# Kernel optimization log

Measured on AMD Instinct MI355X. Metric: run time of the kernel, lower is better.

## Reference

```python
import jax, jax.numpy as jnp
import numpy as np

ANCHOR_LENGTHS = jnp.array([1., 2., 3., 4., 5., 7., 9.], dtype=jnp.float32)  # A = 7


def make_anchors_1d(Lf):
    # anchors [Lf*A, 2] in feature coords, matching torch make_anchors_1d
    centers = jnp.arange(Lf, dtype=jnp.float32) + 0.5          # [Lf]
    c = centers[:, None]                                        # [Lf,1]
    w = ANCHOR_LENGTHS[None, :]                                 # [1,A]
    start = c - 0.5 * w
    end = c + 0.5 * w
    return jnp.stack(jnp.broadcast_arrays(start, end), axis=-1).reshape(-1, 2)


def setup_inputs() -> dict:
    key = jax.random.key(0)
    ks = jax.random.split(key, 4)
    B, C, Lf, A = 8, 512, 16384, 7
    feat = jax.random.normal(ks[0], (B, C, Lf), dtype=jnp.float32)
    conv_w = jax.random.normal(ks[1], (C, C, 3), dtype=jnp.float32) * 0.02
    conv_b = jnp.zeros((C,), dtype=jnp.float32)
    obj_w = jax.random.normal(ks[2], (A, C, 1), dtype=jnp.float32) * 0.02
    obj_b = jnp.zeros((A,), dtype=jnp.float32)
    reg_w = jax.random.normal(ks[3], (A * 2, C, 1), dtype=jnp.float32) * 0.02
    reg_b = jnp.zeros((A * 2,), dtype=jnp.float32)
    return {"feat": feat, "conv_w": conv_w, "conv_b": conv_b,
            "obj_w": obj_w, "obj_b": obj_b, "reg_w": reg_w, "reg_b": reg_b}


def reference(feat, conv_w, conv_b, obj_w, obj_b, reg_w, reg_b):
    B, C, Lf = feat.shape
    A = obj_w.shape[0]
    # conv1d k=3 pad=1 (NCH layout), + bias, relu
    h = jax.lax.conv_general_dilated(
        feat, conv_w, window_strides=(1,), padding=((1, 1),),
        dimension_numbers=("NCH", "OIH", "NCH"))
    h = jax.nn.relu(h + conv_b[None, :, None])                  # [B,C,Lf]
    # 1x1 heads as channel contractions
    obj = jnp.einsum("bcl,ac->bla", h, obj_w[:, :, 0]) + obj_b  # [B,Lf,A]
    reg = jnp.einsum("bcl,oc->blo", h, reg_w[:, :, 0]) + reg_b  # [B,Lf,2A]
    obj = obj.reshape(B, Lf * A)                                # [B,N]
    reg = reg.reshape(B, Lf, A, 2).reshape(B, Lf * A, 2)        # [B,N,2]
    anchors = make_anchors_1d(Lf)                               # [N,2]
    return obj, reg, anchors
```

## Files before the change

kernel.cpp:

```cpp
#include <hip/hip_runtime.h>
#include <hip/hip_bf16.h>
#include <stdint.h>

typedef __attribute__((ext_vector_type(8))) short bh8;
typedef __attribute__((ext_vector_type(4))) float f32x4;
typedef unsigned short u16;
typedef unsigned int u32;

#define B_    8
#define C_    512
#define LF    16384
#define KTOT  1536

#define P4_BYTES ((size_t)4 * B_ * 21 * LF * 4)
#define W2_OFF   P4_BYTES

#define OBJ_OFF  0
#define REG_OFF  917504
#define ANC_OFF  2752512

__device__ __forceinline__ u16 f2bf(float f) {
    u32 u = __float_as_uint(f);
    return (u16)((u + 0x7FFFu + ((u >> 16) & 1u)) >> 16);
}
__device__ __forceinline__ u32 pk2bf(float lo, float hi) {
    u32 r;
    asm("v_cvt_pk_bf16_f32 %0, %1, %2" : "=v"(r) : "v"(lo), "v"(hi));
    return r;
}
__device__ __forceinline__ void gload16(const u16* g, u16* l) {
    __builtin_amdgcn_global_load_lds(
        (const __attribute__((address_space(1))) void*)g,
        (__attribute__((address_space(3))) void*)l, 16, 0, 0);
}

__global__ void k_cast_w(const float* __restrict__ cw, u16* __restrict__ W2) {
    int i = blockIdx.x * 256 + threadIdx.x;
    if (i >= C_ * KTOT) return;
    int co = i / KTOT, r = i % KTOT;
    int t = r >> 9, rem = r & 511;
    int kc = rem >> 6, cc = rem & 63;
    int jl = (cc >> 3) ^ (co & 7);
    int ci = kc * 64 + jl * 8 + (cc & 7);
    W2[i] = f2bf(cw[(co * C_ + ci) * 3 + t]);
}

__global__ void k_anchors(float* __restrict__ out) {
    int l = blockIdx.x * 256 + threadIdx.x;
    if (l >= LF) return;
    const float AL[7] = {1.f, 2.f, 3.f, 4.f, 5.f, 7.f, 9.f};
    float c = (float)l + 0.5f;
    float* an = out + ANC_OFF + (size_t)l * 14;
#pragma unroll
    for (int a = 0; a < 7; ++a) {
        an[a * 2 + 0] = c - 0.5f * AL[a];
        an[a * 2 + 1] = c + 0.5f * AL[a];
    }
}

__global__ __launch_bounds__(256, 4) void k_conv_head(
    const float* __restrict__ feat, const u16* __restrict__ W2,
    const float* __restrict__ conv_b, const float* __restrict__ obj_w,
    const float* __restrict__ reg_w, float* __restrict__ P4) {
    __shared__ __align__(16) char smem[40960];
    u16* As = (u16*)smem;
    u16* Bs = (u16*)(smem + 16384);
    u16* Hs = (u16*)smem;
    u16* Wp = (u16*)(smem + 32768);

    const int tid = threadIdx.x;
    const int lane = tid & 63, wave = tid >> 6;
    const int wm = wave >> 1, wn = wave & 1;
    const int g = lane >> 4, cL = lane & 15;

    const int wg = (blockIdx.x & 7) * 512 + (blockIdx.x >> 3);
    const int mt = wg & 3;
    const int l0 = ((wg >> 2) & 127) * 128;
    const int b  = wg >> 9;
    const int co0 = mt * 128;

    const int cg   = tid & 15;
    const int lgrp = tid >> 4;
    const int arow = tid >> 3;
    const int acol = (tid & 7) * 8;
    const int swA = (cL & 7) << 3;

    f32x4 acc[4][4];
#pragma unroll
    for (int m = 0; m < 4; ++m)
#pragma unroll
        for (int n = 0; n < 4; ++n) acc[m][n] = {0.f, 0.f, 0.f, 0.f};

    for (int kc = 0; kc < 8; ++kc) {
        __syncthreads();
        {
            const float* fp = feat +
                ((size_t)(b * C_ + kc * 64 + cg * 4)) * LF + l0 + lgrp * 8;
#pragma unroll
            for (int h = 0; h < 2; ++h) {
                float4 v0 = *(const float4*)(fp + 0 * LF + h * 4);
                float4 v1 = *(const float4*)(fp + 1 * LF + h * 4);
                float4 v2 = *(const float4*)(fp + 2 * LF + h * 4);
                float4 v3 = *(const float4*)(fp + 3 * LF + h * 4);
#pragma unroll
                for (int e = 0; e < 4; ++e) {
                    const int r = 1 + lgrp * 8 + h * 4 + e;
                    uint2 pk;
                    pk.x = pk2bf(((const float*)&v0)[e], ((const float*)&v1)[e]);
                    pk.y = pk2bf(((const float*)&v2)[e], ((const float*)&v3)[e]);
                    *(uint2*)&Bs[r * 64 + ((cg * 4) ^ ((r & 7) << 3))] = pk;
                }
            }
        }
        if (tid < 128) {
            const int ci2 = tid >> 1;
            const int rr = (tid & 1) ? 129 : 0;
            const int l = l0 + rr - 1;
            float v = (l >= 0 && l < LF)
                          ? feat[((size_t)(b * C_ + kc * 64 + ci2)) * LF + l]
                          : 0.f;
            Bs[rr * 64 + (ci2 ^ ((rr & 7) << 3))] = f2bf(v);
        }
#pragma unroll
        for (int t = 0; t < 3; ++t) {
            if (t > 0) __syncthreads();
#pragma unroll
            for (int p = 0; p < 4; ++p) {
                const int row = p * 32 + arow;
                gload16(&W2[(size_t)(co0 + row) * KTOT + t * 512 + kc * 64 + acol],
                        &As[row * 64 + acol]);
            }
            __syncthreads();
            const int swB = ((cL + t) & 7) << 3;
#pragma unroll
            for (int kk = 0; kk < 2; ++kk) {
                const int ko = kk * 32 + g * 8;
                bh8 af[4], bfr[4];
#pragma unroll
                for (int m = 0; m < 4; ++m)
                    af[m] = *(const bh8*)&As[(wm * 64 + m * 16 + cL) * 64 + (ko ^ swA)];
#pragma unroll
                for (int n = 0; n < 4; ++n)
                    bfr[n] = *(const bh8*)&Bs[(wn * 64 + n * 16 + cL + t) * 64 + (ko ^ swB)];
#pragma unroll
                for (int m = 0; m < 4; ++m)
#pragma unroll
                    for (int n = 0; n < 4; ++n)
                        acc[m][n] = __builtin_amdgcn_mfma_f32_16x16x32_bf16(
                            af[m], bfr[n], acc[m][n], 0, 0, 0);
            }
        }
    }
    __syncthreads();

#pragma unroll
    for (int m = 0; m < 4; ++m) {
        const int co_b = wm * 64 + m * 16 + g * 4;
        const float b0_ = conv_b[co0 + co_b + 0];
        const float b1_ = conv_b[co0 + co_b + 1];
        const float b2_ = conv_b[co0 + co_b + 2];
        const float b3_ = conv_b[co0 + co_b + 3];
#pragma unroll
        for (int n = 0; n < 4; ++n) {
            const int l = wn * 64 + n * 16 + cL;
            f32x4 v = acc[m][n];
            uint2 pk;
            pk.x = pk2bf(fmaxf(v[0] + b0_, 0.f), fmaxf(v[1] + b1_, 0.f));
            pk.y = pk2bf(fmaxf(v[2] + b2_, 0.f), fmaxf(v[3] + b3_, 0.f));
            *(uint2*)&Hs[l * 128 + (co_b ^ ((cL & 7) << 3))] = pk;
        }
    }
#pragma unroll
    for (int it = 0; it < 4; ++it) {
        const int q = it * 256 + tid;
        const int a = q >> 5, c0 = (q & 31) * 4;
        float4 wv = {0.f, 0.f, 0.f, 0.f};
        if (a < 7)       wv = *(const float4*)&obj_w[a * C_ + co0 + c0];
        else if (a < 21) wv = *(const float4*)&reg_w[(a - 7) * C_ + co0 + c0];
        uint2 pk;
        pk.x = pk2bf(wv.x, wv.y);
        pk.y = pk2bf(wv.z, wv.w);
        *(uint2*)&Wp[a * 128 + (c0 ^ ((a & 7) << 3))] = pk;
    }
    __syncthreads();

    f32x4 hacc[2][2];
#pragma unroll
    for (int m = 0; m < 2; ++m)
#pragma unroll
        for (int n = 0; n < 2; ++n) hacc[m][n] = {0.f, 0.f, 0.f, 0.f};
    const int ln0 = wave * 32;
#pragma unroll
    for (int ks2 = 0; ks2 < 4; ++ks2) {
        const int ko = ks2 * 32 + g * 8;
        bh8 wa[2], hb[2];
        wa[0] = *(const bh8*)&Wp[cL * 128 + (ko ^ swA)];
        wa[1] = *(const bh8*)&Wp[(16 + cL) * 128 + (ko ^ swA)];
        hb[0] = *(const bh8*)&Hs[(ln0 + cL) * 128 + (ko ^ swA)];
        hb[1] = *(const bh8*)&Hs[(ln0 + 16 + cL) * 128 + (ko ^ swA)];
#pragma unroll
        for (int m = 0; m < 2; ++m)
#pragma unroll
            for (int n = 0; n < 2; ++n)
                hacc[m][n] = __builtin_amdgcn_mfma_f32_16x16x32_bf16(
                    wa[m], hb[n], hacc[m][n], 0, 0, 0);
    }
    float* P4base = P4 + ((size_t)(mt * B_ + b) * 21) * LF + l0;
#pragma unroll
    for (int m = 0; m < 2; ++m) {
        const int a0 = m * 16 + g * 4;
#pragma unroll
        for (int n = 0; n < 2; ++n) {
            const int l = ln0 + n * 16 + cL;
#pragma unroll
            for (int r = 0; r < 4; ++r) {
                const int a = a0 + r;
                if (a < 21) P4base[(size_t)a * LF + l] = hacc[m][n][r];
            }
        }
    }
}

__global__ void k_finalize(const float* __restrict__ P4, const float* __restrict__ obj_b,
                           const float* __restrict__ reg_b, float* __restrict__ out) {
    int gid = blockIdx.x * 256 + threadIdx.x;
    if (gid >= B_ * LF) return;
    int b = gid >> 14, l = gid & (LF - 1);
    float s[21];
#pragma unroll
    for (int a = 0; a < 21; ++a) {
        float v = 0.f;
#pragma unroll
        for (int m = 0; m < 4; ++m) v += P4[((size_t)(m * B_ + b) * 21 + a) * LF + l];
        s[a] = v;
    }
    float* op = out + OBJ_OFF + (size_t)b * (LF * 7) + (size_t)l * 7;
#pragma unroll
    for (int a = 0; a < 7; ++a) op[a] = s[a] + obj_b[a];
    float* rp = out + REG_OFF + (size_t)b * (LF * 14) + (size_t)l * 14;
#pragma unroll
    for (int o = 0; o < 14; ++o) rp[o] = s[7 + o] + reg_b[o];
}

extern "C" void kernel_launch(void* const* d_in, const int* in_sizes, int n_in,
                              void* d_out, int out_size, void* d_ws, size_t ws_size,
                              hipStream_t stream) {
    const float* feat   = (const float*)d_in[0];
    const float* conv_w = (const float*)d_in[1];
    const float* conv_b = (const float*)d_in[2];
    const float* obj_w  = (const float*)d_in[3];
    const float* obj_b  = (const float*)d_in[4];
    const float* reg_w  = (const float*)d_in[5];
    const float* reg_b  = (const float*)d_in[6];
    char* ws = (char*)d_ws;
    float* P4 = (float*)ws;
    u16* W2   = (u16*)(ws + W2_OFF);
    float* out = (float*)d_out;

    k_cast_w<<<3072, 256, 0, stream>>>(conv_w, W2);
    k_anchors<<<64, 256, 0, stream>>>(out);
    k_conv_head<<<4096, 256, 0, stream>>>(feat, W2, conv_b, obj_w, reg_w, P4);
    k_finalize<<<(B_ * LF + 255) / 256, 256, 0, stream>>>(P4, obj_b, reg_b, out);
}
```

Measured before the change: 266.1 us.

## Double-buffer weight tiles and prefetch features in a 512-thread conv block

Enlarges the conv tile to 256 sequence positions using 512 threads (8 waves) and moves shared memory to a dynamic allocation. Weight tiles for all three taps of the next channel chunk are loaded asynchronously into a second LDS buffer. Features are prefetched into registers while the current chunk runs its MFMAs, which removes the per-tap barriers. MFMA sections are also raised in wave priority. The cost is about 128KB of LDS per block, which allows only one block per CU and lowers wave occupancy.

Measured after the change: 267.0 us. About the same (+0.3%).

```diff
diff --git a/kernel.cpp b/kernel.cpp
--- a/kernel.cpp
+++ b/kernel.cpp
@@ -18,6 +18,8 @@
 #define OBJ_OFF  0
 #define REG_OFF  917504
 #define ANC_OFF  2752512
+
+#define SMEM_BYTES 131328
 
 __device__ __forceinline__ u16 f2bf(float f) {
     u32 u = __float_as_uint(f);
@@ -58,31 +60,27 @@
     }
 }
 
-__global__ __launch_bounds__(256, 4) void k_conv_head(
+__global__ __launch_bounds__(512, 2) void k_conv_head(
     const float* __restrict__ feat, const u16* __restrict__ W2,
     const float* __restrict__ conv_b, const float* __restrict__ obj_w,
     const float* __restrict__ reg_w, float* __restrict__ P4) {
-    __shared__ __align__(16) char smem[40960];
-    u16* As = (u16*)smem;
-    u16* Bs = (u16*)(smem + 16384);
+    extern __shared__ __align__(16) char smem[];
+    u16* Bs = (u16*)(smem + 98304);
     u16* Hs = (u16*)smem;
-    u16* Wp = (u16*)(smem + 32768);
+    u16* Wp = (u16*)(smem + 65536);
 
     const int tid = threadIdx.x;
     const int lane = tid & 63, wave = tid >> 6;
-    const int wm = wave >> 1, wn = wave & 1;
+    const int wm = wave >> 2, wn = wave & 3;
     const int g = lane >> 4, cL = lane & 15;
 
-    const int wg = (blockIdx.x & 7) * 512 + (blockIdx.x >> 3);
+    const int wg = (blockIdx.x & 7) * 256 + (blockIdx.x >> 3);
     const int mt = wg & 3;
-    const int l0 = ((wg >> 2) & 127) * 128;
-    const int b  = wg >> 9;
+    const int l0 = ((wg >> 2) & 63) * 256;
+    const int b  = wg >> 8;
     const int co0 = mt * 128;
 
-    const int cg   = tid & 15;
-    const int lgrp = tid >> 4;
-    const int arow = tid >> 3;
-    const int acol = (tid & 7) * 8;
+    const int cg = tid & 15, lgrp = tid >> 4;
     const int swA = (cL & 7) << 3;
 
     f32x4 acc[4][4];
@@ -90,47 +88,65 @@
     for (int m = 0; m < 4; ++m)
 #pragma unroll
         for (int n = 0; n < 4; ++n) acc[m][n] = {0.f, 0.f, 0.f, 0.f};
+
+    float4 fv[2][4];
+    float hvf = 0.f;
+    const int haloci = tid >> 1;
+    const int halol  = l0 + ((tid & 1) ? 256 : -1);
+    const int halorr = (tid & 1) ? 257 : 0;
+
+#define LOADB(kcv)                                                              \
+    {                                                                           \
+        const float* fp = feat +                                                \
+            ((size_t)(b * C_ + (kcv) * 64 + cg * 4)) * LF + l0 + lgrp * 8;      \
+        _Pragma("unroll")                                                       \
+        for (int h = 0; h < 2; ++h)                                             \
+            _Pragma("unroll")                                                   \
+            for (int j = 0; j < 4; ++j)                                         \
+                fv[h][j] = *(const float4*)(fp + j * LF + h * 4);               \
+        if (tid < 128)                                                          \
+            hvf = (halol >= 0 && halol < LF)                                    \
+                ? feat[((size_t)(b * C_ + (kcv) * 64 + haloci)) * LF + halol]   \
+                : 0.f;                                                          \
+    }
+
+#define ISSUEA(kcv, buf)                                                        \
+    {                                                                           \
+        u16* Ab_ = (u16*)(smem + (buf) * 49152);                                \
+        _Pragma("unroll")                                                       \
+        for (int t = 0; t < 3; ++t)                                             \
+            _Pragma("unroll")                                                   \
+            for (int p = 0; p < 2; ++p)                                         \
+                gload16(&W2[(size_t)(co0 + p * 64 + (tid >> 3)) * KTOT +        \
+                            t * 512 + (kcv) * 64 + (tid & 7) * 8],              \
+                        &Ab_[t * 8192 + p * 4096 + tid * 8]);                   \
+    }
+
+    ISSUEA(0, 0)
+    LOADB(0)
 
     for (int kc = 0; kc < 8; ++kc) {
         __syncthreads();
-        {
-            const float* fp = feat +
-                ((size_t)(b * C_ + kc * 64 + cg * 4)) * LF + l0 + lgrp * 8;
-#pragma unroll
-            for (int h = 0; h < 2; ++h) {
-                float4 v0 = *(const float4*)(fp + 0 * LF + h * 4);
-                float4 v1 = *(const float4*)(fp + 1 * LF + h * 4);
-                float4 v2 = *(const float4*)(fp + 2 * LF + h * 4);
-                float4 v3 = *(const float4*)(fp + 3 * LF + h * 4);
-#pragma unroll
-                for (int e = 0; e < 4; ++e) {
-                    const int r = 1 + lgrp * 8 + h * 4 + e;
-                    uint2 pk;
-                    pk.x = pk2bf(((const float*)&v0)[e], ((const float*)&v1)[e]);
-                    pk.y = pk2bf(((const float*)&v2)[e], ((const float*)&v3)[e]);
-                    *(uint2*)&Bs[r * 64 + ((cg * 4) ^ ((r & 7) << 3))] = pk;
-                }
+#pragma unroll
+        for (int h = 0; h < 2; ++h)
+#pragma unroll
+            for (int e = 0; e < 4; ++e) {
+                const int r = 1 + lgrp * 8 + h * 4 + e;
+                uint2 pk;
+                pk.x = pk2bf(((const float*)&fv[h][0])[e], ((const float*)&fv[h][1])[e]);
+                pk.y = pk2bf(((const float*)&fv[h][2])[e], ((const float*)&fv[h][3])[e]);
+                *(uint2*)&Bs[r * 64 + ((cg * 4) ^ ((r & 7) << 3))] = pk;
             }
-        }
-        if (tid < 128) {
-            const int ci2 = tid >> 1;
-            const int rr = (tid & 1) ? 129 : 0;
-            const int l = l0 + rr - 1;
-            float v = (l >= 0 && l < LF)
-                          ? feat[((size_t)(b * C_ + kc * 64 + ci2)) * LF + l]
-                          : 0.f;
-            Bs[rr * 64 + (ci2 ^ ((rr & 7) << 3))] = f2bf(v);
-        }
+        if (tid < 128)
+            Bs[halorr * 64 + (haloci ^ ((halorr & 7) << 3))] = f2bf(hvf);
+        __syncthreads();
+        if (kc < 7) {
+            ISSUEA(kc + 1, (kc + 1) & 1)
+            LOADB(kc + 1)
+        }
+        u16* Ab = (u16*)(smem + (kc & 1) * 49152);
 #pragma unroll
         for (int t = 0; t < 3; ++t) {
-            if (t > 0) __syncthreads();
-#pragma unroll
-            for (int p = 0; p < 4; ++p) {
-                const int row = p * 32 + arow;
-                gload16(&W2[(size_t)(co0 + row) * KTOT + t * 512 + kc * 64 + acol],
-                        &As[row * 64 + acol]);
-            }
-            __syncthreads();
             const int swB = ((cL + t) & 7) << 3;
 #pragma unroll
             for (int kk = 0; kk < 2; ++kk) {
@@ -138,16 +154,18 @@
                 bh8 af[4], bfr[4];
 #pragma unroll
                 for (int m = 0; m < 4; ++m)
-                    af[m] = *(const bh8*)&As[(wm * 64 + m * 16 + cL) * 64 + (ko ^ swA)];
+                    af[m] = *(const bh8*)&Ab[t * 8192 + (wm * 64 + m * 16 + cL) * 64 + (ko ^ swA)];
 #pragma unroll
                 for (int n = 0; n < 4; ++n)
                     bfr[n] = *(const bh8*)&Bs[(wn * 64 + n * 16 + cL + t) * 64 + (ko ^ swB)];
+                __builtin_amdgcn_s_setprio(1);
 #pragma unroll
                 for (int m = 0; m < 4; ++m)
 #pragma unroll
                     for (int n = 0; n < 4; ++n)
                         acc[m][n] = __builtin_amdgcn_mfma_f32_16x16x32_bf16(
                             af[m], bfr[n], acc[m][n], 0, 0, 0);
+                __builtin_amdgcn_s_setprio(0);
             }
         }
     }
@@ -171,8 +189,8 @@
         }
     }
 #pragma unroll
-    for (int it = 0; it < 4; ++it) {
-        const int q = it * 256 + tid;
+    for (int it = 0; it < 2; ++it) {
+        const int q = it * 512 + tid;
         const int a = q >> 5, c0 = (q & 31) * 4;
         float4 wv = {0.f, 0.f, 0.f, 0.f};
         if (a < 7)       wv = *(const float4*)&obj_w[a * C_ + co0 + c0];
@@ -257,8 +275,11 @@
     u16* W2   = (u16*)(ws + W2_OFF);
     float* out = (float*)d_out;
 
+    hipFuncSetAttribute((const void*)k_conv_head,
+                        hipFuncAttributeMaxDynamicSharedMemorySize, SMEM_BYTES);
+
     k_cast_w<<<3072, 256, 0, stream>>>(conv_w, W2);
     k_anchors<<<64, 256, 0, stream>>>(out);
-    k_conv_head<<<4096, 256, 0, stream>>>(feat, W2, conv_b, obj_w, reg_w, P4);
+    k_conv_head<<<2048, 512, SMEM_BYTES, stream>>>(feat, W2, conv_b, obj_w, reg_w, P4);
     k_finalize<<<(B_ * LF + 255) / 256, 256, 0, stream>>>(P4, obj_b, reg_b, out);
 }
```

## Switch conv GEMM operands from bf16 to fp8 and stage all three taps at once

Applied to the files above, without the earlier changes.

Converts the conv weights and the feature tile to fp8 (e4m3) and uses fp8 MFMA instructions instead of bf16 ones, halving the operand bytes in LDS and global memory. The weight tiles for all three conv taps are now loaded together per k-chunk, which removes two barriers per chunk. The aim is higher MFMA throughput and less LDS and memory traffic. The cost is a large loss of precision in the activations and weights, which may break tolerance against the fp32 reference.

New measurement: 243.4 us. 1.09x faster.

```diff
diff --git a/kernel.cpp b/kernel.cpp
--- a/kernel.cpp
+++ b/kernel.cpp
@@ -2,10 +2,10 @@
 #include <hip/hip_bf16.h>
 #include <stdint.h>
 
-typedef __attribute__((ext_vector_type(8))) short bh8;
 typedef __attribute__((ext_vector_type(4))) float f32x4;
 typedef unsigned short u16;
 typedef unsigned int u32;
+typedef unsigned char u8;
 
 #define B_    8
 #define C_    512
@@ -13,7 +13,7 @@
 #define KTOT  1536
 
 #define P4_BYTES ((size_t)4 * B_ * 21 * LF * 4)
-#define W2_OFF   P4_BYTES
+#define W8_OFF   P4_BYTES
 
 #define OBJ_OFF  0
 #define REG_OFF  917504
@@ -28,21 +28,24 @@
     asm("v_cvt_pk_bf16_f32 %0, %1, %2" : "=v"(r) : "v"(lo), "v"(hi));
     return r;
 }
-__device__ __forceinline__ void gload16(const u16* g, u16* l) {
+__device__ __forceinline__ void gload16(const u8* g, u8* l) {
     __builtin_amdgcn_global_load_lds(
         (const __attribute__((address_space(1))) void*)g,
         (__attribute__((address_space(3))) void*)l, 16, 0, 0);
 }
 
-__global__ void k_cast_w(const float* __restrict__ cw, u16* __restrict__ W2) {
+__global__ void k_cast_w(const float* __restrict__ cw, u8* __restrict__ W8) {
     int i = blockIdx.x * 256 + threadIdx.x;
-    if (i >= C_ * KTOT) return;
-    int co = i / KTOT, r = i % KTOT;
-    int t = r >> 9, rem = r & 511;
+    if (i >= C_ * KTOT / 2) return;
+    int co = i / (KTOT / 2), r = (i % (KTOT / 2)) * 2;
+    int t = r / 512, rem = r % 512;
     int kc = rem >> 6, cc = rem & 63;
     int jl = (cc >> 3) ^ (co & 7);
     int ci = kc * 64 + jl * 8 + (cc & 7);
-    W2[i] = f2bf(cw[(co * C_ + ci) * 3 + t]);
+    float f0 = cw[(co * C_ + ci) * 3 + t];
+    float f1 = cw[(co * C_ + ci + 1) * 3 + t];
+    u32 pk = __builtin_amdgcn_cvt_pk_fp8_f32(f0, f1, 0, false);
+    *(u16*)&W8[(size_t)co * KTOT + r] = (u16)pk;
 }
 
 __global__ void k_anchors(float* __restrict__ out) {
@@ -59,12 +62,12 @@
 }
 
 __global__ __launch_bounds__(256, 4) void k_conv_head(
-    const float* __restrict__ feat, const u16* __restrict__ W2,
+    const float* __restrict__ feat, const u8* __restrict__ W8,
     const float* __restrict__ conv_b, const float* __restrict__ obj_w,
     const float* __restrict__ reg_w, float* __restrict__ P4) {
     __shared__ __align__(16) char smem[40960];
-    u16* As = (u16*)smem;
-    u16* Bs = (u16*)(smem + 16384);
+    u8* As3 = (u8*)smem;
+    u8* Bs  = (u8*)(smem + 24576);
     u16* Hs = (u16*)smem;
     u16* Wp = (u16*)(smem + 32768);
 
@@ -79,11 +82,8 @@
     const int b  = wg >> 9;
     const int co0 = mt * 128;
 
-    const int cg   = tid & 15;
-    const int lgrp = tid >> 4;
-    const int arow = tid >> 3;
-    const int acol = (tid & 7) * 8;
-    const int swA = (cL & 7) << 3;
+    const int cg = tid & 15, lgrp = tid >> 4;
+    const int swA8 = (cL & 7) << 3;
 
     f32x4 acc[4][4];
 #pragma unroll
@@ -105,48 +105,53 @@
 #pragma unroll
                 for (int e = 0; e < 4; ++e) {
                     const int r = 1 + lgrp * 8 + h * 4 + e;
-                    uint2 pk;
-                    pk.x = pk2bf(((const float*)&v0)[e], ((const float*)&v1)[e]);
-                    pk.y = pk2bf(((const float*)&v2)[e], ((const float*)&v3)[e]);
-                    *(uint2*)&Bs[r * 64 + ((cg * 4) ^ ((r & 7) << 3))] = pk;
+                    u32 w0 = __builtin_amdgcn_cvt_pk_fp8_f32(
+                        ((const float*)&v0)[e], ((const float*)&v1)[e], 0, false);
+                    u32 w  = __builtin_amdgcn_cvt_pk_fp8_f32(
+                        ((const float*)&v2)[e], ((const float*)&v3)[e], w0, true);
+                    *(u32*)&Bs[r * 64 + ((cg * 4) ^ ((r & 7) << 3))] = w;
                 }
             }
         }
         if (tid < 128) {
             const int ci2 = tid >> 1;
             const int rr = (tid & 1) ? 129 : 0;
-            const int l = l0 + rr - 1;
+            const int l = l0 + ((tid & 1) ? 128 : -1);
             float v = (l >= 0 && l < LF)
                           ? feat[((size_t)(b * C_ + kc * 64 + ci2)) * LF + l]
                           : 0.f;
-            Bs[rr * 64 + (ci2 ^ ((rr & 7) << 3))] = f2bf(v);
-        }
+            u32 p = __builtin_amdgcn_cvt_pk_fp8_f32(v, 0.f, 0, false);
+            Bs[rr * 64 + (ci2 ^ ((rr & 7) << 3))] = (u8)p;
+        }
+#pragma unroll
+        for (int t = 0; t < 3; ++t)
+#pragma unroll
+            for (int p = 0; p < 2; ++p) {
+                const int row = p * 64 + (tid >> 2);
+                const int colB = (tid & 3) * 16;
+                gload16(&W8[(size_t)(co0 + row) * KTOT + t * 512 + kc * 64 + colB],
+                        &As3[t * 8192 + row * 64 + colB]);
+            }
+        __syncthreads();
 #pragma unroll
         for (int t = 0; t < 3; ++t) {
-            if (t > 0) __syncthreads();
-#pragma unroll
-            for (int p = 0; p < 4; ++p) {
-                const int row = p * 32 + arow;
-                gload16(&W2[(size_t)(co0 + row) * KTOT + t * 512 + kc * 64 + acol],
-                        &As[row * 64 + acol]);
-            }
-            __syncthreads();
-            const int swB = ((cL + t) & 7) << 3;
+            const u8* At = As3 + t * 8192;
+            const int swB8 = ((cL + t) & 7) << 3;
 #pragma unroll
             for (int kk = 0; kk < 2; ++kk) {
                 const int ko = kk * 32 + g * 8;
-                bh8 af[4], bfr[4];
+                long af[4], bfr[4];
 #pragma unroll
                 for (int m = 0; m < 4; ++m)
-                    af[m] = *(const bh8*)&As[(wm * 64 + m * 16 + cL) * 64 + (ko ^ swA)];
+                    af[m] = *(const long*)&At[(wm * 64 + m * 16 + cL) * 64 + (ko ^ swA8)];
 #pragma unroll
                 for (int n = 0; n < 4; ++n)
-                    bfr[n] = *(const bh8*)&Bs[(wn * 64 + n * 16 + cL + t) * 64 + (ko ^ swB)];
+                    bfr[n] = *(const long*)&Bs[(wn * 64 + n * 16 + cL + t) * 64 + (ko ^ swB8)];
 #pragma unroll
                 for (int m = 0; m < 4; ++m)
 #pragma unroll
                     for (int n = 0; n < 4; ++n)
-                        acc[m][n] = __builtin_amdgcn_mfma_f32_16x16x32_bf16(
+                        acc[m][n] = __builtin_amdgcn_mfma_f32_16x16x32_fp8_fp8(
                             af[m], bfr[n], acc[m][n], 0, 0, 0);
             }
         }
@@ -184,12 +189,14 @@
     }
     __syncthreads();
 
+    typedef __attribute__((ext_vector_type(8))) short bh8;
     f32x4 hacc[2][2];
 #pragma unroll
     for (int m = 0; m < 2; ++m)
 #pragma unroll
         for (int n = 0; n < 2; ++n) hacc[m][n] = {0.f, 0.f, 0.f, 0.f};
     const int ln0 = wave * 32;
+    const int swA = (cL & 7) << 3;
 #pragma unroll
     for (int ks2 = 0; ks2 < 4; ++ks2) {
         const int ko = ks2 * 32 + g * 8;
@@ -254,11 +261,11 @@
     const float* reg_b  = (const float*)d_in[6];
     char* ws = (char*)d_ws;
     float* P4 = (float*)ws;
-    u16* W2   = (u16*)(ws + W2_OFF);
+    u8* W8    = (u8*)(ws + W8_OFF);
     float* out = (float*)d_out;
 
-    k_cast_w<<<3072, 256, 0, stream>>>(conv_w, W2);
+    k_cast_w<<<1536, 256, 0, stream>>>(conv_w, W8);
     k_anchors<<<64, 256, 0, stream>>>(out);
-    k_conv_head<<<4096, 256, 0, stream>>>(feat, W2, conv_b, obj_w, reg_w, P4);
+    k_conv_head<<<4096, 256, 0, stream>>>(feat, W8, conv_b, obj_w, reg_w, P4);
     k_finalize<<<(B_ * LF + 255) / 256, 256, 0, stream>>>(P4, obj_b, reg_b, out);
 }
```
